# Optimization experiments

Measured on AMD Instinct MI355X. Metric: run time of the kernel, lower is better.

The kernel has to match this reference:

```python
import jax, jax.numpy as jnp
import numpy as np

N = 50000          # nodes
E = 500000         # edges
EMB = 64           # hidden_size
R = 2              # DDE num_rounds
RR = 2             # DDE num_reverse_rounds
PRED_IN = 4 * EMB + 4 + 4 * (R + RR)  # 276


def setup_inputs() -> dict:
    key = jax.random.key(0)
    ks = jax.random.split(key, 10)
    x = jax.random.normal(ks[0], (N, EMB), jnp.float32)
    edge_index = jax.random.randint(ks[1], (2, E), 0, N, dtype=jnp.int64)
    edge_attr = jax.random.normal(ks[2], (E, EMB), jnp.float32)
    topic_signal = jax.random.uniform(ks[3], (N, 2), dtype=jnp.float32)
    q_emb = jax.random.normal(ks[4], (E, EMB), jnp.float32)
    # learned parameters
    non_text_emb = jax.random.normal(ks[5], (1, EMB), jnp.float32)
    W1 = jax.random.normal(ks[6], (PRED_IN, EMB), jnp.float32) / np.sqrt(PRED_IN)
    b1 = jnp.zeros((EMB,), jnp.float32)
    W2 = jax.random.normal(ks[7], (EMB, 1), jnp.float32) / np.sqrt(EMB)
    b2 = jnp.zeros((1,), jnp.float32)
    return dict(x=x, edge_index=edge_index, edge_attr=edge_attr,
                topic_signal=topic_signal, q_emb=q_emb,
                non_text_emb=non_text_emb, W1=W1, b1=b1, W2=W2, b2=b2)


def _segment_mean(data, seg, num_segments):
    # mean aggregation as in PyG MessagePassing(aggr='mean'); empty segments -> 0
    s = jax.ops.segment_sum(data, seg, num_segments=num_segments)
    cnt = jax.ops.segment_sum(jnp.ones((seg.shape[0],), data.dtype), seg,
                              num_segments=num_segments)
    return s / jnp.maximum(cnt, 1.0)[:, None]


def reference(x, edge_index, edge_attr, topic_signal, q_emb,
              non_text_emb, W1, b1, W2, b2):
    src, dst = edge_index[0], edge_index[1]
    # replace all-zero node rows with the learned non-text entity embedding
    zero_mask = jnp.all(x == 0, axis=1)
    x = jnp.where(zero_mask[:, None], non_text_emb[0], x)

    feats = [x, topic_signal]  # topic_pe = True
    # DDE forward rounds: aggregate src -> dst along edge_index
    h = topic_signal
    for _ in range(R):
        h = _segment_mean(h[src], dst, N)
        feats.append(h)
    # DDE reverse rounds: flipped edges (dst -> src)
    h = topic_signal
    for _ in range(RR):
        h = _segment_mean(h[dst], src, N)
        feats.append(h)

    h_e = jnp.concatenate(feats, axis=1)                      # [N, EMB+2+2*(R+RR)]
    h_triple = jnp.concatenate([q_emb, h_e[src], edge_attr, h_e[dst]], axis=1)  # [E, PRED_IN]
    hidden = jax.nn.relu(h_triple @ W1 + b1)                  # [E, EMB]
    return (hidden @ W2 + b2).squeeze(-1)                     # [E]
```

## Files before the change

kernel.cpp:

```cpp
#include <hip/hip_runtime.h>
#include <cstdint>
#include <cstddef>


typedef __bf16 bf16x8 __attribute__((ext_vector_type(8)));
typedef float f32x4 __attribute__((ext_vector_type(4)));

__device__ __forceinline__ unsigned int f2bf1(float f) {
    unsigned int u = __float_as_uint(f);
    return (u + 0x7fffu + ((u >> 16) & 1u)) >> 16;
}
__device__ __forceinline__ unsigned int pk2(float a, float b) {
    return f2bf1(a) | (f2bf1(b) << 16);
}
__device__ __forceinline__ bf16x8 cvt8(const float* __restrict__ p) {
    float4 v0 = *(const float4*)p;
    float4 v1 = *(const float4*)(p + 4);
    bf16x8 r;
    r[0] = (__bf16)v0.x; r[1] = (__bf16)v0.y; r[2] = (__bf16)v0.z; r[3] = (__bf16)v0.w;
    r[4] = (__bf16)v1.x; r[5] = (__bf16)v1.y; r[6] = (__bf16)v1.z; r[7] = (__bf16)v1.w;
    return r;
}


__global__ void k_detect(const int* __restrict__ idx, int E, int* __restrict__ flag) {
    int e = blockIdx.x * blockDim.x + threadIdx.x;
    bool nz = (e < E) && (idx[2 * e + 1] != 0);
    unsigned long long m = __ballot(nz);
    if (m != 0ull && (threadIdx.x & 63) == 0) atomicOr(flag, 1);
}

__global__ void k_convert(const int* __restrict__ idx, int E, const int* __restrict__ flag,
                          int* __restrict__ src_i, int* __restrict__ dst_i,
                          int* __restrict__ cnt_dst, int* __restrict__ cnt_src,
                          unsigned short* __restrict__ pos_f, unsigned short* __restrict__ pos_r) {
    int e = blockIdx.x * blockDim.x + threadIdx.x;
    if (e >= E) return;
    int s, d;
    if (*flag) { s = idx[e];     d = idx[E + e]; }
    else       { s = idx[2 * e]; d = idx[2 * E + 2 * e]; }
    src_i[e] = s; dst_i[e] = d;
    pos_f[e] = (unsigned short)atomicAdd(&cnt_dst[d], 1);
    pos_r[e] = (unsigned short)atomicAdd(&cnt_src[s], 1);
}

__global__ void k_scan(const int* __restrict__ cnt_dst, const int* __restrict__ cnt_src,
                       int* __restrict__ off_f, int* __restrict__ off_r, int N) {
    const int* cnt = (blockIdx.x == 0) ? cnt_dst : cnt_src;
    int* off       = (blockIdx.x == 0) ? off_f   : off_r;
    const int t = threadIdx.x;
    const int C = (N + 1023) / 1024;
    int lo = t * C, hi = lo + C; if (hi > N) hi = N; if (lo > N) lo = N;
    int sum = 0;
    for (int i = lo; i < hi; ++i) sum += cnt[i];
    __shared__ int wsum[16];
    int lane = t & 63, wv = t >> 6;
    int v = sum;
    for (int ofs = 1; ofs < 64; ofs <<= 1) {
        int u = __shfl_up(v, ofs);
        if (lane >= ofs) v += u;
    }
    if (lane == 63) wsum[wv] = v;
    __syncthreads();
    if (wv == 0) {
        int x = (lane < 16) ? wsum[lane] : 0;
        for (int ofs = 1; ofs < 16; ofs <<= 1) {
            int u = __shfl_up(x, ofs);
            if (lane >= ofs) x += u;
        }
        if (lane < 16) wsum[lane] = x;
    }
    __syncthreads();
    int base = (wv > 0 ? wsum[wv - 1] : 0) + (v - sum);
    for (int i = lo; i < hi; ++i) { off[i] = base; base += cnt[i]; }
}

__global__ void k_fill(const int* __restrict__ src_i, const int* __restrict__ dst_i,
                       const unsigned short* __restrict__ pos_f, const unsigned short* __restrict__ pos_r,
                       const int* __restrict__ off_f, const int* __restrict__ off_r,
                       int* __restrict__ csr_f, int* __restrict__ csr_r, int E) {
    int e = blockIdx.x * blockDim.x + threadIdx.x;
    if (e >= E) return;
    int s = src_i[e], d = dst_i[e];
    csr_f[off_f[d] + pos_f[e]] = s;
    csr_r[off_r[s] + pos_r[e]] = d;
}

__global__ void k_round(const int* __restrict__ off_f, const int* __restrict__ csr_f,
                        const int* __restrict__ off_r, const int* __restrict__ csr_r,
                        const float* __restrict__ hf_in,
                        const float* __restrict__ hr_in,
                        float* __restrict__ f_out, float* __restrict__ r_out,
                        int N, int E) {
    int n = blockIdx.x * blockDim.x + threadIdx.x;
    if (n >= N) return;
    const float2* hf = (const float2*)hf_in;
    const float2* hr = (const float2*)hr_in;
    {
        int b = off_f[n], e = (n + 1 < N) ? off_f[n + 1] : E;
        float sx = 0.f, sy = 0.f;
        for (int j = b; j < e; ++j) { float2 t = hf[csr_f[j]]; sx += t.x; sy += t.y; }
        float inv = 1.0f / (float)max(e - b, 1);
        ((float2*)f_out)[n] = make_float2(sx * inv, sy * inv);
    }
    {
        int b = off_r[n], e = (n + 1 < N) ? off_r[n + 1] : E;
        float sx = 0.f, sy = 0.f;
        for (int j = b; j < e; ++j) { float2 t = hr[csr_r[j]]; sx += t.x; sy += t.y; }
        float inv = 1.0f / (float)max(e - b, 1);
        ((float2*)r_out)[n] = make_float2(sx * inv, sy * inv);
    }
}

__global__ void k_build(const float* __restrict__ x, const float* __restrict__ topic,
                        const float* __restrict__ nte,
                        const float* __restrict__ f1, const float* __restrict__ f2,
                        const float* __restrict__ r1, const float* __restrict__ r2,
                        unsigned short* __restrict__ he, int N) {
    int n = blockIdx.x * blockDim.x + threadIdx.x;
    if (n >= N) return;
    const float4* xr = (const float4*)(x + (size_t)n * 64);
    float4 v[16];
    bool allz = true;
#pragma unroll
    for (int i = 0; i < 16; ++i) {
        v[i] = xr[i];
        allz = allz && (v[i].x == 0.f && v[i].y == 0.f && v[i].z == 0.f && v[i].w == 0.f);
    }
    const float4* nr = (const float4*)nte;
    unsigned int row[40];
#pragma unroll
    for (int i = 0; i < 16; ++i) {
        float4 s = allz ? nr[i] : v[i];
        row[2 * i]     = pk2(s.x, s.y);
        row[2 * i + 1] = pk2(s.z, s.w);
    }
    row[32] = pk2(topic[2 * n], topic[2 * n + 1]);
    row[33] = pk2(f1[2 * n], f1[2 * n + 1]);
    row[34] = pk2(f2[2 * n], f2[2 * n + 1]);
    row[35] = pk2(r1[2 * n], r1[2 * n + 1]);
    row[36] = pk2(r2[2 * n], r2[2 * n + 1]);
    row[37] = 0u; row[38] = 0u; row[39] = 0u;
    uint4* dst = (uint4*)(he + (size_t)n * 80);
#pragma unroll
    for (int i = 0; i < 10; ++i) dst[i] = ((const uint4*)row)[i];
}

__global__ void k_w1t(const float* __restrict__ W1, unsigned short* __restrict__ W1T) {
    int i = blockIdx.x * blockDim.x + threadIdx.x;
    if (i >= 64 * 288) return;
    int col = i / 288, pk = i - col * 288;
    int k = 0; bool valid = true;
    if (pk < 64)       { k = pk; }
    else if (pk < 128) { k = 138 + (pk - 64); }
    else if (pk < 208) { int j = pk - 128; k = 64 + j;  valid = j < 74; }
    else               { int j = pk - 208; k = 202 + j; valid = j < 74; }
    float v = valid ? W1[k * 64 + col] : 0.f;
    W1T[col * 288 + pk] = (unsigned short)f2bf1(v);
}


__launch_bounds__(256, 3)
__global__ void k_gemm(const float* __restrict__ q_emb,
                       const float* __restrict__ edge_attr,
                       const unsigned short* __restrict__ he,
                       const unsigned short* __restrict__ W1T,
                       const int* __restrict__ src_i, const int* __restrict__ dst_i,
                       const float* __restrict__ b1, const float* __restrict__ W2,
                       const float* __restrict__ b2, float* __restrict__ out, int E)
{
    const int tid = threadIdx.x;
    const int w = tid >> 6, l = tid & 63, c = l & 15, q = l >> 4;
    const int ebase = blockIdx.x * 256 + w * 64;

    const float* gq[4];
    const float* ga[4];
    const unsigned short* hs[4];
    const unsigned short* hd[4];
#pragma unroll
    for (int t = 0; t < 4; ++t) {
        int ee = ebase + t * 16 + c; ee = ee < E ? ee : E - 1;
        int s = src_i[ee], d = dst_i[ee];
        gq[t] = q_emb     + (size_t)ee * 64 + q * 8;
        ga[t] = edge_attr + (size_t)ee * 64 + q * 8;
        hs[t] = he + (size_t)s * 80 + q * 8;
        hd[t] = he + (size_t)d * 80 + q * 8;
    }

    float b1v[4], w2v[4];
#pragma unroll
    for (int ct = 0; ct < 4; ++ct) { b1v[ct] = b1[ct * 16 + c]; w2v[ct] = W2[ct * 16 + c]; }
    const float bb = b2[0];

    f32x4 acc[4][4] = {};

    const unsigned short* wrow = W1T + (size_t)c * 288 + q * 8;
#define BF(ct, ks) (*(const bf16x8*)(wrow + (ct) * (16 * 288) + (ks) * 32))
#define KSTEP(ks, AEXPR)                                                               \
    {                                                                                  \
        bf16x8 bf0 = BF(0, ks), bf1 = BF(1, ks), bf2 = BF(2, ks), bf3 = BF(3, ks);     \
        _Pragma("unroll")                                                              \
        for (int t = 0; t < 4; ++t) {                                                  \
            bf16x8 a = (AEXPR);                                                        \
            acc[t][0] = __builtin_amdgcn_mfma_f32_16x16x32_bf16(a, bf0, acc[t][0], 0, 0, 0); \
            acc[t][1] = __builtin_amdgcn_mfma_f32_16x16x32_bf16(a, bf1, acc[t][1], 0, 0, 0); \
            acc[t][2] = __builtin_amdgcn_mfma_f32_16x16x32_bf16(a, bf2, acc[t][2], 0, 0, 0); \
            acc[t][3] = __builtin_amdgcn_mfma_f32_16x16x32_bf16(a, bf3, acc[t][3], 0, 0, 0); \
        }                                                                              \
    }

    KSTEP(0, cvt8(gq[t]))
    KSTEP(1, cvt8(gq[t] + 32))
    KSTEP(2, cvt8(ga[t]))
    KSTEP(3, cvt8(ga[t] + 32))
    KSTEP(4, (*(const bf16x8*)(hs[t])))
    KSTEP(5, (*(const bf16x8*)(hs[t] + 32)))
    KSTEP(6, (*(const bf16x8*)((q < 2) ? (hs[t] + 64) : (hd[t] - 16))))
    KSTEP(7, (*(const bf16x8*)(hd[t] + 16)))
    KSTEP(8, (*(const bf16x8*)(hd[t] + 48)))
#undef KSTEP
#undef BF

#pragma unroll
    for (int t = 0; t < 4; ++t) {
        float pr[4];
#pragma unroll
        for (int r = 0; r < 4; ++r) {
            float h0 = fmaxf(acc[t][0][r] + b1v[0], 0.f);
            float h1 = fmaxf(acc[t][1][r] + b1v[1], 0.f);
            float h2 = fmaxf(acc[t][2][r] + b1v[2], 0.f);
            float h3 = fmaxf(acc[t][3][r] + b1v[3], 0.f);
            float p = fmaf(h0, w2v[0], fmaf(h1, w2v[1], fmaf(h2, w2v[2], h3 * w2v[3])));
            p += __shfl_xor(p, 1);
            p += __shfl_xor(p, 2);
            p += __shfl_xor(p, 4);
            p += __shfl_xor(p, 8);
            pr[r] = p;
        }
        if (c == 0) {
            int eo = ebase + t * 16 + q * 4;
            if (eo < E) {
                float4 o = make_float4(pr[0] + bb, pr[1] + bb, pr[2] + bb, pr[3] + bb);
                *(float4*)&out[eo] = o;
            }
        }
    }
}


extern "C" void kernel_launch(void* const* d_in, const int* in_sizes, int n_in,
                              void* d_out, int out_size, void* d_ws, size_t ws_size,
                              hipStream_t stream)
{
    const float* x         = (const float*)d_in[0];
    const int*   eidx      = (const int*)  d_in[1];
    const float* edge_attr = (const float*)d_in[2];
    const float* topic     = (const float*)d_in[3];
    const float* q_emb     = (const float*)d_in[4];
    const float* nte       = (const float*)d_in[5];
    const float* W1        = (const float*)d_in[6];
    const float* b1        = (const float*)d_in[7];
    const float* W2        = (const float*)d_in[8];
    const float* b2        = (const float*)d_in[9];
    float* out = (float*)d_out;

    const int E = out_size;
    const int N = in_sizes[0] / 64;

    char* ws = (char*)d_ws;
    int* flag  = (int*)ws;
    int* src_i = (int*)(ws + 16);
    int* dst_i = src_i + E;
    int* off_f = dst_i + E;
    int* off_r = off_f + N;
    float* fblk = (float*)(off_r + N);
    float* f1 = fblk;
    float* f2 = fblk + 2 * (size_t)N;
    float* r1 = fblk + 4 * (size_t)N;
    float* r2 = fblk + 6 * (size_t)N;
    int* cnt_dst = (int*)f1;
    int* cnt_src = cnt_dst + N;
    char* heblk = (char*)(fblk + 8 * (size_t)N);
    unsigned short* pos_f = (unsigned short*)heblk;
    unsigned short* pos_r = pos_f + E;
    int* csr_f = (int*)(pos_r + E);
    int* csr_r = csr_f + E;
    unsigned short* he = (unsigned short*)heblk;
    size_t he_bytes = (size_t)N * 160;
    size_t trans_bytes = (size_t)E * 12;
    size_t heblk_bytes = he_bytes > trans_bytes ? he_bytes : trans_bytes;
    unsigned short* W1T = (unsigned short*)(heblk + heblk_bytes);

    size_t needed = 16 + (size_t)8 * E + (size_t)8 * N + (size_t)32 * N + heblk_bytes + 64 * 288 * 2;
    if (ws_size < needed) return;

    hipMemsetAsync(flag, 0, 16, stream);
    hipMemsetAsync(cnt_dst, 0, (size_t)8 * N, stream);

    const int gE = (E + 255) / 256;
    const int gN = (N + 255) / 256;

    k_detect <<<gE, 256, 0, stream>>>(eidx, E, flag);
    k_convert<<<gE, 256, 0, stream>>>(eidx, E, flag, src_i, dst_i,
                                      cnt_dst, cnt_src, pos_f, pos_r);
    k_scan   <<<2, 1024, 0, stream>>>(cnt_dst, cnt_src, off_f, off_r, N);
    k_fill   <<<gE, 256, 0, stream>>>(src_i, dst_i, pos_f, pos_r, off_f, off_r,
                                      csr_f, csr_r, E);
    k_round  <<<gN, 256, 0, stream>>>(off_f, csr_f, off_r, csr_r, topic, topic, f1, r1, N, E);
    k_round  <<<gN, 256, 0, stream>>>(off_f, csr_f, off_r, csr_r, f1, r1, f2, r2, N, E);
    k_build  <<<gN, 256, 0, stream>>>(x, topic, nte, f1, f2, r1, r2, he, N);
    k_w1t    <<<(64 * 288 + 255) / 256, 256, 0, stream>>>(W1, W1T);

    k_gemm<<<(E + 255) / 256, 256, 0, stream>>>(q_emb, edge_attr, he, W1T,
                                                src_i, dst_i, b1, W2, b2, out, E);
}
```

Measured before the change: 599.7 us.

## Prefetch GEMM operands, shrink edge tile, parallelize CSR rounds with subgroups

The edge GEMM now loads all A fragments for two 16-edge tiles up front, halving edges per block from 256 to 128, and double-buffers W1T fragments across the K steps so more loads are in flight before the MFMAs. The DDE round kernel assigns 16 lanes per node with a shuffle reduction instead of one thread per node, to cut the serial neighbor loop and load imbalance. CSR fill switches from per-edge stored positions to atomic cursors, which drops the pos arrays but makes neighbor order nondeterministic, so float summation order can vary between runs. The higher register use from preloading A may reduce occupancy.

```diff
diff --git a/kernel.cpp b/kernel.cpp
--- a/kernel.cpp
+++ b/kernel.cpp
@@ -32,22 +32,23 @@
 
 __global__ void k_convert(const int* __restrict__ idx, int E, const int* __restrict__ flag,
                           int* __restrict__ src_i, int* __restrict__ dst_i,
-                          int* __restrict__ cnt_dst, int* __restrict__ cnt_src,
-                          unsigned short* __restrict__ pos_f, unsigned short* __restrict__ pos_r) {
+                          int* __restrict__ cnt_dst, int* __restrict__ cnt_src) {
     int e = blockIdx.x * blockDim.x + threadIdx.x;
     if (e >= E) return;
     int s, d;
     if (*flag) { s = idx[e];     d = idx[E + e]; }
     else       { s = idx[2 * e]; d = idx[2 * E + 2 * e]; }
     src_i[e] = s; dst_i[e] = d;
-    pos_f[e] = (unsigned short)atomicAdd(&cnt_dst[d], 1);
-    pos_r[e] = (unsigned short)atomicAdd(&cnt_src[s], 1);
+    atomicAdd(&cnt_dst[d], 1);
+    atomicAdd(&cnt_src[s], 1);
 }
 
 __global__ void k_scan(const int* __restrict__ cnt_dst, const int* __restrict__ cnt_src,
-                       int* __restrict__ off_f, int* __restrict__ off_r, int N) {
+                       int* __restrict__ off_f, int* __restrict__ off_r,
+                       int* __restrict__ cur_f, int* __restrict__ cur_r, int N) {
     const int* cnt = (blockIdx.x == 0) ? cnt_dst : cnt_src;
     int* off       = (blockIdx.x == 0) ? off_f   : off_r;
+    int* cur       = (blockIdx.x == 0) ? cur_f   : cur_r;
     const int t = threadIdx.x;
     const int C = (N + 1023) / 1024;
     int lo = t * C, hi = lo + C; if (hi > N) hi = N; if (lo > N) lo = N;
@@ -72,43 +73,54 @@
     }
     __syncthreads();
     int base = (wv > 0 ? wsum[wv - 1] : 0) + (v - sum);
-    for (int i = lo; i < hi; ++i) { off[i] = base; base += cnt[i]; }
+    for (int i = lo; i < hi; ++i) { off[i] = base; cur[i] = base; base += cnt[i]; }
 }
 
 __global__ void k_fill(const int* __restrict__ src_i, const int* __restrict__ dst_i,
-                       const unsigned short* __restrict__ pos_f, const unsigned short* __restrict__ pos_r,
-                       const int* __restrict__ off_f, const int* __restrict__ off_r,
+                       int* __restrict__ cur_f, int* __restrict__ cur_r,
                        int* __restrict__ csr_f, int* __restrict__ csr_r, int E) {
     int e = blockIdx.x * blockDim.x + threadIdx.x;
     if (e >= E) return;
     int s = src_i[e], d = dst_i[e];
-    csr_f[off_f[d] + pos_f[e]] = s;
-    csr_r[off_r[s] + pos_r[e]] = d;
+    csr_f[atomicAdd(&cur_f[d], 1)] = s;
+    csr_r[atomicAdd(&cur_r[s], 1)] = d;
 }
 
 __global__ void k_round(const int* __restrict__ off_f, const int* __restrict__ csr_f,
                         const int* __restrict__ off_r, const int* __restrict__ csr_r,
-                        const float* __restrict__ hf_in,
-                        const float* __restrict__ hr_in,
+                        const float* __restrict__ hf_in, const float* __restrict__ hr_in,
                         float* __restrict__ f_out, float* __restrict__ r_out,
                         int N, int E) {
-    int n = blockIdx.x * blockDim.x + threadIdx.x;
+    int n   = blockIdx.x * 16 + (threadIdx.x >> 4);
+    int sub = threadIdx.x & 15;
     if (n >= N) return;
     const float2* hf = (const float2*)hf_in;
     const float2* hr = (const float2*)hr_in;
     {
-        int b = off_f[n], e = (n + 1 < N) ? off_f[n + 1] : E;
+        int b = off_f[n], en = (n + 1 < N) ? off_f[n + 1] : E;
         float sx = 0.f, sy = 0.f;
-        for (int j = b; j < e; ++j) { float2 t = hf[csr_f[j]]; sx += t.x; sy += t.y; }
-        float inv = 1.0f / (float)max(e - b, 1);
-        ((float2*)f_out)[n] = make_float2(sx * inv, sy * inv);
+        for (int j = b + sub; j < en; j += 16) { float2 t = hf[csr_f[j]]; sx += t.x; sy += t.y; }
+        sx += __shfl_xor(sx, 1); sy += __shfl_xor(sy, 1);
+        sx += __shfl_xor(sx, 2); sy += __shfl_xor(sy, 2);
+        sx += __shfl_xor(sx, 4); sy += __shfl_xor(sy, 4);
+        sx += __shfl_xor(sx, 8); sy += __shfl_xor(sy, 8);
+        if (sub == 0) {
+            float inv = 1.0f / (float)max(en - b, 1);
+            ((float2*)f_out)[n] = make_float2(sx * inv, sy * inv);
+        }
     }
     {
-        int b = off_r[n], e = (n + 1 < N) ? off_r[n + 1] : E;
+        int b = off_r[n], en = (n + 1 < N) ? off_r[n + 1] : E;
         float sx = 0.f, sy = 0.f;
-        for (int j = b; j < e; ++j) { float2 t = hr[csr_r[j]]; sx += t.x; sy += t.y; }
-        float inv = 1.0f / (float)max(e - b, 1);
-        ((float2*)r_out)[n] = make_float2(sx * inv, sy * inv);
+        for (int j = b + sub; j < en; j += 16) { float2 t = hr[csr_r[j]]; sx += t.x; sy += t.y; }
+        sx += __shfl_xor(sx, 1); sy += __shfl_xor(sy, 1);
+        sx += __shfl_xor(sx, 2); sy += __shfl_xor(sy, 2);
+        sx += __shfl_xor(sx, 4); sy += __shfl_xor(sy, 4);
+        sx += __shfl_xor(sx, 8); sy += __shfl_xor(sy, 8);
+        if (sub == 0) {
+            float inv = 1.0f / (float)max(en - b, 1);
+            ((float2*)r_out)[n] = make_float2(sx * inv, sy * inv);
+        }
     }
 }
 
@@ -171,20 +183,26 @@
 {
     const int tid = threadIdx.x;
     const int w = tid >> 6, l = tid & 63, c = l & 15, q = l >> 4;
-    const int ebase = blockIdx.x * 256 + w * 64;
-
-    const float* gq[4];
-    const float* ga[4];
-    const unsigned short* hs[4];
-    const unsigned short* hd[4];
-#pragma unroll
-    for (int t = 0; t < 4; ++t) {
+    const int ebase = blockIdx.x * 128 + w * 32;
+
+    bf16x8 A[2][9];
+#pragma unroll
+    for (int t = 0; t < 2; ++t) {
         int ee = ebase + t * 16 + c; ee = ee < E ? ee : E - 1;
         int s = src_i[ee], d = dst_i[ee];
-        gq[t] = q_emb     + (size_t)ee * 64 + q * 8;
-        ga[t] = edge_attr + (size_t)ee * 64 + q * 8;
-        hs[t] = he + (size_t)s * 80 + q * 8;
-        hd[t] = he + (size_t)d * 80 + q * 8;
+        const float* gq = q_emb     + (size_t)ee * 64 + q * 8;
+        const float* ga = edge_attr + (size_t)ee * 64 + q * 8;
+        const unsigned short* phs = he + (size_t)s * 80 + q * 8;
+        const unsigned short* phd = he + (size_t)d * 80 + q * 8;
+        A[t][0] = cvt8(gq);
+        A[t][1] = cvt8(gq + 32);
+        A[t][2] = cvt8(ga);
+        A[t][3] = cvt8(ga + 32);
+        A[t][4] = *(const bf16x8*)(phs);
+        A[t][5] = *(const bf16x8*)(phs + 32);
+        A[t][6] = *(const bf16x8*)((q < 2) ? (phs + 64) : (phd - 16));
+        A[t][7] = *(const bf16x8*)(phd + 16);
+        A[t][8] = *(const bf16x8*)(phd + 48);
     }
 
     float b1v[4], w2v[4];
@@ -192,37 +210,34 @@
     for (int ct = 0; ct < 4; ++ct) { b1v[ct] = b1[ct * 16 + c]; w2v[ct] = W2[ct * 16 + c]; }
     const float bb = b2[0];
 
-    f32x4 acc[4][4] = {};
-
+    f32x4 acc[2][4] = {};
     const unsigned short* wrow = W1T + (size_t)c * 288 + q * 8;
-#define BF(ct, ks) (*(const bf16x8*)(wrow + (ct) * (16 * 288) + (ks) * 32))
-#define KSTEP(ks, AEXPR)                                                               \
-    {                                                                                  \
-        bf16x8 bf0 = BF(0, ks), bf1 = BF(1, ks), bf2 = BF(2, ks), bf3 = BF(3, ks);     \
-        _Pragma("unroll")                                                              \
-        for (int t = 0; t < 4; ++t) {                                                  \
-            bf16x8 a = (AEXPR);                                                        \
-            acc[t][0] = __builtin_amdgcn_mfma_f32_16x16x32_bf16(a, bf0, acc[t][0], 0, 0, 0); \
-            acc[t][1] = __builtin_amdgcn_mfma_f32_16x16x32_bf16(a, bf1, acc[t][1], 0, 0, 0); \
-            acc[t][2] = __builtin_amdgcn_mfma_f32_16x16x32_bf16(a, bf2, acc[t][2], 0, 0, 0); \
-            acc[t][3] = __builtin_amdgcn_mfma_f32_16x16x32_bf16(a, bf3, acc[t][3], 0, 0, 0); \
-        }                                                                              \
-    }
-
-    KSTEP(0, cvt8(gq[t]))
-    KSTEP(1, cvt8(gq[t] + 32))
-    KSTEP(2, cvt8(ga[t]))
-    KSTEP(3, cvt8(ga[t] + 32))
-    KSTEP(4, (*(const bf16x8*)(hs[t])))
-    KSTEP(5, (*(const bf16x8*)(hs[t] + 32)))
-    KSTEP(6, (*(const bf16x8*)((q < 2) ? (hs[t] + 64) : (hd[t] - 16))))
-    KSTEP(7, (*(const bf16x8*)(hd[t] + 16)))
-    KSTEP(8, (*(const bf16x8*)(hd[t] + 48)))
-#undef KSTEP
-#undef BF
-
-#pragma unroll
-    for (int t = 0; t < 4; ++t) {
+
+    bf16x8 Bn[4];
+#pragma unroll
+    for (int ct = 0; ct < 4; ++ct) Bn[ct] = *(const bf16x8*)(wrow + ct * (16 * 288));
+
+#pragma unroll
+    for (int ks = 0; ks < 9; ++ks) {
+        bf16x8 Bc[4];
+#pragma unroll
+        for (int ct = 0; ct < 4; ++ct) Bc[ct] = Bn[ct];
+        if (ks < 8) {
+#pragma unroll
+            for (int ct = 0; ct < 4; ++ct)
+                Bn[ct] = *(const bf16x8*)(wrow + ct * (16 * 288) + (ks + 1) * 32);
+        }
+#pragma unroll
+        for (int t = 0; t < 2; ++t) {
+#pragma unroll
+            for (int ct = 0; ct < 4; ++ct)
+                acc[t][ct] = __builtin_amdgcn_mfma_f32_16x16x32_bf16(A[t][ks], Bc[ct],
+                                                                     acc[t][ct], 0, 0, 0);
+        }
+    }
+
+#pragma unroll
+    for (int t = 0; t < 2; ++t) {
         float pr[4];
 #pragma unroll
         for (int r = 0; r < 4; ++r) {
@@ -268,30 +283,30 @@
     const int N = in_sizes[0] / 64;
 
     char* ws = (char*)d_ws;
-    int* flag  = (int*)ws;
-    int* src_i = (int*)(ws + 16);
-    int* dst_i = src_i + E;
-    int* off_f = dst_i + E;
-    int* off_r = off_f + N;
-    float* fblk = (float*)(off_r + N);
-    float* f1 = fblk;
-    float* f2 = fblk + 2 * (size_t)N;
-    float* r1 = fblk + 4 * (size_t)N;
-    float* r2 = fblk + 6 * (size_t)N;
-    int* cnt_dst = (int*)f1;
+    int* flag    = (int*)ws;
+    int* src_i   = (int*)(ws + 16);
+    int* dst_i   = src_i + E;
+    int* cnt_dst = dst_i + E;
     int* cnt_src = cnt_dst + N;
-    char* heblk = (char*)(fblk + 8 * (size_t)N);
-    unsigned short* pos_f = (unsigned short*)heblk;
-    unsigned short* pos_r = pos_f + E;
-    int* csr_f = (int*)(pos_r + E);
+    int* off_f   = cnt_src + N;
+    int* off_r   = off_f + N;
+    int* cur_f   = off_r + N;
+    int* cur_r   = cur_f + N;
+    float* f1 = (float*)(cur_r + N);
+    float* f2 = f1 + 2 * (size_t)N;
+    float* r1 = f2 + 2 * (size_t)N;
+    float* r2 = r1 + 2 * (size_t)N;
+    char* heblk = (char*)(r2 + 2 * (size_t)N);
+    int* csr_f = (int*)heblk;
     int* csr_r = csr_f + E;
     unsigned short* he = (unsigned short*)heblk;
     size_t he_bytes = (size_t)N * 160;
-    size_t trans_bytes = (size_t)E * 12;
-    size_t heblk_bytes = he_bytes > trans_bytes ? he_bytes : trans_bytes;
+    size_t csr_bytes = (size_t)E * 8;
+    size_t heblk_bytes = he_bytes > csr_bytes ? he_bytes : csr_bytes;
     unsigned short* W1T = (unsigned short*)(heblk + heblk_bytes);
 
-    size_t needed = 16 + (size_t)8 * E + (size_t)8 * N + (size_t)32 * N + heblk_bytes + 64 * 288 * 2;
+    size_t needed = 16 + (size_t)8 * E + (size_t)24 * N + (size_t)32 * N
+                  + heblk_bytes + 64 * 288 * 2;
     if (ws_size < needed) return;
 
     hipMemsetAsync(flag, 0, 16, stream);
@@ -299,18 +314,17 @@
 
     const int gE = (E + 255) / 256;
     const int gN = (N + 255) / 256;
+    const int gRN = (N + 15) / 16;
 
     k_detect <<<gE, 256, 0, stream>>>(eidx, E, flag);
-    k_convert<<<gE, 256, 0, stream>>>(eidx, E, flag, src_i, dst_i,
-                                      cnt_dst, cnt_src, pos_f, pos_r);
-    k_scan   <<<2, 1024, 0, stream>>>(cnt_dst, cnt_src, off_f, off_r, N);
-    k_fill   <<<gE, 256, 0, stream>>>(src_i, dst_i, pos_f, pos_r, off_f, off_r,
-                                      csr_f, csr_r, E);
-    k_round  <<<gN, 256, 0, stream>>>(off_f, csr_f, off_r, csr_r, topic, topic, f1, r1, N, E);
-    k_round  <<<gN, 256, 0, stream>>>(off_f, csr_f, off_r, csr_r, f1, r1, f2, r2, N, E);
+    k_convert<<<gE, 256, 0, stream>>>(eidx, E, flag, src_i, dst_i, cnt_dst, cnt_src);
+    k_scan   <<<2, 1024, 0, stream>>>(cnt_dst, cnt_src, off_f, off_r, cur_f, cur_r, N);
+    k_fill   <<<gE, 256, 0, stream>>>(src_i, dst_i, cur_f, cur_r, csr_f, csr_r, E);
+    k_round  <<<gRN, 256, 0, stream>>>(off_f, csr_f, off_r, csr_r, topic, topic, f1, r1, N, E);
+    k_round  <<<gRN, 256, 0, stream>>>(off_f, csr_f, off_r, csr_r, f1, r1, f2, r2, N, E);
     k_build  <<<gN, 256, 0, stream>>>(x, topic, nte, f1, f2, r1, r2, he, N);
     k_w1t    <<<(64 * 288 + 255) / 256, 256, 0, stream>>>(W1, W1T);
 
-    k_gemm<<<(E + 255) / 256, 256, 0, stream>>>(q_emb, edge_attr, he, W1T,
+    k_gemm<<<(E + 127) / 128, 256, 0, stream>>>(q_emb, edge_attr, he, W1T,
                                                 src_i, dst_i, b1, W2, b2, out, E);
 }
```

Result: slower. 679.3 us (+13.3%).
